# Performance work log

Hardware: AMD Instinct MI355X
Metric: run time of the kernel (lower is better)

## Reference

```python
import jax, jax.numpy as jnp
import numpy as np
from jax import lax

CONF_THRESH = 0.65
NMS_THRESH = 0.55
EPS = 1e-16


def setup_inputs() -> dict:
    key = jax.random.key(0)
    x = jax.random.uniform(key, (8, 4096, 85), dtype=jnp.float32)
    return {"x": x}


def _xywh2xyxy(b):
    # b: [..., 4] center-x, center-y, w, h -> x1, y1, x2, y2
    cx, cy, w, h = b[..., 0], b[..., 1], b[..., 2], b[..., 3]
    return jnp.stack([cx - w / 2, cy - h / 2, cx + w / 2, cy + h / 2], axis=-1)


def _pairwise_iou(boxes):
    # boxes: [bs, N, 4] in xyxy -> iou: [bs, N, N]
    x1, y1, x2, y2 = boxes[..., 0], boxes[..., 1], boxes[..., 2], boxes[..., 3]
    ix1 = jnp.maximum(x1[:, :, None], x1[:, None, :])
    iy1 = jnp.maximum(y1[:, :, None], y1[:, None, :])
    ix2 = jnp.minimum(x2[:, :, None], x2[:, None, :])
    iy2 = jnp.minimum(y2[:, :, None], y2[:, None, :])
    inter = jnp.clip(ix2 - ix1, 0.0) * jnp.clip(iy2 - iy1, 0.0)
    area = (x2 - x1) * (y2 - y1)
    return inter / (area[:, :, None] + area[:, None, :] - inter + EPS)


def reference(x):
    # x: [bs, N, 5 + nC]
    bs, N, _ = x.shape
    obj = x[..., 4]
    valid = obj > CONF_THRESH                      # foreground filter
    boxes = _xywh2xyxy(x[..., :4])
    max_conf = jnp.max(x[..., 5:], axis=-1)        # per-box best class score
    cls_idx = jnp.argmax(x[..., 5:], axis=-1)

    # sort descending by class confidence (invalid boxes pushed to the end)
    sort_key = jnp.where(valid, max_conf, -jnp.inf)
    order = jnp.argsort(-sort_key, axis=1)         # [bs, N]
    boxes_s = jnp.take_along_axis(boxes, order[..., None], axis=1)
    obj_s = jnp.take_along_axis(obj, order, axis=1)
    conf_s = jnp.take_along_axis(max_conf, order, axis=1)
    cls_s = jnp.take_along_axis(cls_idx, order, axis=1)
    valid_s = jnp.take_along_axis(valid, order, axis=1)

    # candidate suppression matrix: same class AND IoU above threshold
    iou = _pairwise_iou(boxes_s)                   # [bs, N, N]
    same_cls = cls_s[:, :, None] == cls_s[:, None, :]
    sup_mat = (iou > NMS_THRESH) & same_cls        # [bs, N, N]

    # greedy sequential NMS over boxes in descending-score order
    def step(suppressed, xs):
        sup_row, vld, i = xs                       # sup_row: [bs, N], vld: [bs]
        keep_i = vld & ~suppressed[:, i]
        suppressed = suppressed | (keep_i[:, None] & sup_row)
        return suppressed, keep_i

    xs = (jnp.swapaxes(sup_mat, 0, 1), valid_s.T, jnp.arange(N))
    _, keeps = lax.scan(step, jnp.zeros((bs, N), dtype=bool), xs)
    keep = keeps.T                                 # [bs, N]

    # [batch_idx, x1, y1, x2, y2, p_obj, max_conf, cls_idx]; non-kept rows zeroed
    batch_idx = jnp.broadcast_to(
        jnp.arange(bs, dtype=x.dtype)[:, None, None], (bs, N, 1))
    preds = jnp.concatenate(
        [batch_idx, boxes_s, obj_s[..., None], conf_s[..., None],
         cls_s[..., None].astype(x.dtype)], axis=-1)  # [bs, N, 8]
    return preds * keep[..., None].astype(x.dtype)
```

## Files before the change

kernel.cpp:

```cpp
#include <hip/hip_runtime.h>

constexpr int BS = 8;
constexpr int N  = 4096;
constexpr int F  = 85;
constexpr int NC = 80;
constexpr float CONF_T = 0.65f;
constexpr float NMS_T  = 0.55f;
constexpr int MC   = 96;
constexpr int SEGS = 32;
constexpr int SEGR = 128;


__global__ __launch_bounds__(256) void prep_kernel(
        const float* __restrict__ x,
        unsigned long long* __restrict__ gkeys,
        float4* __restrict__ vbox,
        float2* __restrict__ vco,
        int* __restrict__ cntblk,
        float4* __restrict__ out) {
    __shared__ __align__(16) float sx[SEGR * F];
    __shared__ float sbest2[SEGR];
    __shared__ int   sbi2[SEGR];
    __shared__ int   wq[4];
    const int tid = threadIdx.x, blk = blockIdx.x;
    const int row0 = blk * SEGR;
    const float4* src = (const float4*)(x + (size_t)row0 * F);
    float4* dst = (float4*)sx;
    constexpr int NV4 = SEGR * F / 4;
    for (int i = tid; i < NV4; i += 256) dst[i] = src[i];
    out[(size_t)row0 * 2 + tid] = make_float4(0.f, 0.f, 0.f, 0.f);
    __syncthreads();

    const int r = tid & 127, h = tid >> 7;
    float mybest; int mybi;
    {
        const float* p = sx + r * F + 5 + h * 40;
        float best = p[0]; int bi = 0;
        #pragma unroll 8
        for (int c = 1; c < 40; ++c) {
            float v = p[c];
            if (v > best) { best = v; bi = c; }
        }
        mybest = best; mybi = bi + h * 40;
        if (h) { sbest2[r] = best; sbi2[r] = mybi; }
    }
    __syncthreads();

    bool valid = false;
    unsigned long long key = 0;
    if (!h) {
        float b1 = sbest2[r];
        if (b1 > mybest) { mybest = b1; mybi = sbi2[r]; }
        const float* p = sx + r * F;
        float obj = p[4];
        valid = obj > CONF_T;
        const int t = row0 + r;
        if (valid) {
            float cx = p[0], cy = p[1], w = p[2], hh = p[3];
            vbox[t] = make_float4(cx - w * 0.5f, cy - hh * 0.5f,
                                  cx + w * 0.5f, cy + hh * 0.5f);
            vco[t]  = make_float2(obj, mybest);
        }
        key = ((unsigned long long)(~__float_as_uint(mybest)) << 19)
            | ((unsigned long long)(unsigned)(t & (N - 1)) << 7)
            | (unsigned)mybi;
    }
    const int lane = tid & 63, w = tid >> 6;
    unsigned long long mask = __ballot(valid);
    if (lane == 0) wq[w] = __popcll(mask);
    __syncthreads();
    int base = 0;
    for (int i = 0; i < w; ++i) base += wq[i];
    if (valid) {
        int slot = base + __popcll(mask & ((1ull << lane) - 1ull));
        gkeys[((size_t)(blk >> 5) << 12) + ((blk & 31) << 7) + slot] = key;
    }
    if (tid == 0) cntblk[blk] = wq[0] + wq[1];
}

__global__ __launch_bounds__(256) void rank_kernel(
        const unsigned long long* __restrict__ gkeys,
        const float4* __restrict__ vbox,
        const float2* __restrict__ vco,
        const int* __restrict__ cntblk,
        float4* __restrict__ rbox,
        float2* __restrict__ rco,
        int* __restrict__ rcls,
        int* __restrict__ cnt) {
    __shared__ __align__(16) unsigned long long sk[N + 2];
    __shared__ int scnt[SEGS];
    __shared__ int soff[SEGS];
    __shared__ int snv;
    __shared__ int part[256];
    const int b = blockIdx.y, tid = threadIdx.x;
    if (tid < SEGS) {
        int v = cntblk[b * SEGS + tid];
        int xx = v;
        #pragma unroll
        for (int d = 1; d < SEGS; d <<= 1) {
            int y = __shfl_up(xx, d);
            if (tid >= d) xx += y;
        }
        scnt[tid] = v;
        soff[tid] = xx - v;
        if (tid == SEGS - 1) snv = xx;
    }
    __syncthreads();
    const int nv = snv;
    if (blockIdx.x == 0 && tid == 0) cnt[b] = nv;
    const int c0 = blockIdx.x * 64;
    if (c0 >= nv) return;

    const unsigned long long* kb = gkeys + ((size_t)b << 12);
    #pragma unroll 4
    for (int g = tid; g < SEGS * SEGR; g += 256) {
        int s = g >> 7, j = g & 127;
        if (j < scnt[s]) sk[soff[s] + j] = kb[g];
    }
    if (tid == 0) { sk[nv] = ~0ull; sk[nv + 1] = ~0ull; }
    __syncthreads();

    const int li = tid & 63, q = tid >> 6;
    const int bi = c0 + li;
    const bool active = bi < nv;
    const unsigned long long myk = active ? sk[bi] : 0;
    const int P = (nv + 1) >> 1;
    const int j0 = (P * q) >> 2, j1 = (P * (q + 1)) >> 2;
    const ulonglong2* skp = (const ulonglong2*)sk;
    int cr = 0;
    for (int j = j0; j < j1; ++j) {
        ulonglong2 kk = skp[j];
        cr += (kk.x < myk) ? 1 : 0;
        cr += (kk.y < myk) ? 1 : 0;
    }
    part[tid] = cr;
    __syncthreads();
    if (q == 0 && active) {
        int rank = part[li] + part[li + 64] + part[li + 128] + part[li + 192];
        int idx = (int)((myk >> 7) & (N - 1));
        int s = (b << 12) + idx;
        int d = (b << 12) + rank;
        rbox[d] = vbox[s];
        rco[d]  = vco[s];
        rcls[d] = (int)(myk & 127u);
    }
}

__global__ __launch_bounds__(64) void nms_kernel(
        const float4* __restrict__ rbox,
        const float2* __restrict__ rco,
        const int* __restrict__ rcls,
        const int* __restrict__ cnt,
        float4* __restrict__ out) {
    __shared__ float4 sbox[MC];
    __shared__ unsigned short srank[MC];
    __shared__ unsigned char srem[MC];
    const int c = blockIdx.x, b = blockIdx.y, lane = threadIdx.x;
    const int bN = b << 12;
    const int nv = cnt[b];
    constexpr int MAXCH = 32;

    int cv[MAXCH];
    #pragma unroll
    for (int ch = 0; ch < MAXCH; ++ch) {
        int rn = ch * 64 + lane;
        cv[ch] = rcls[bN + (rn < nv ? rn : 0)];
    }
    int n = 0;
    #pragma unroll
    for (int ch = 0; ch < MAXCH; ++ch) {
        int rn = ch * 64 + lane;
        bool member = (rn < nv) && (cv[ch] == c);
        unsigned long long mb = __ballot(member);
        if (member) {
            int pos = n + __popcll(mb & ((1ull << lane) - 1ull));
            if (pos < MC) srank[pos] = (unsigned short)rn;
        }
        n += __popcll(mb);
    }
    for (int base = MAXCH * 64; base < nv; base += 64) {
        int rn = base + lane;
        bool member = (rn < nv) && (rcls[bN + (rn < nv ? rn : 0)] == c);
        unsigned long long mb = __ballot(member);
        if (member) {
            int pos = n + __popcll(mb & ((1ull << lane) - 1ull));
            if (pos < MC) srank[pos] = (unsigned short)rn;
        }
        n += __popcll(mb);
    }
    if (n > MC) n = MC;
    const int m = n;

    for (int i = lane; i < m; i += 64) {
        sbox[i] = rbox[bN + srank[i]];
        srem[i] = 0;
    }

    for (int i = 0; i < m; ++i) {
        if (srem[i]) continue;
        float4 bi4 = sbox[i];
        float ai = (bi4.z - bi4.x) * (bi4.w - bi4.y);
        for (int j = i + 1 + lane; j < m; j += 64) {
            if (!srem[j]) {
                float4 bj = sbox[j];
                float ix1 = fmaxf(bi4.x, bj.x);
                float iy1 = fmaxf(bi4.y, bj.y);
                float ix2 = fminf(bi4.z, bj.z);
                float iy2 = fminf(bi4.w, bj.w);
                float inter = fmaxf(ix2 - ix1, 0.0f) * fmaxf(iy2 - iy1, 0.0f);
                float aj = (bj.z - bj.x) * (bj.w - bj.y);
                float iou = inter / (ai + aj - inter + 1e-16f);
                if (iou > NMS_T) srem[j] = 1;
            }
        }
    }
    for (int j = lane; j < m; j += 64) {
        if (!srem[j]) {
            int rr = srank[j];
            float4 bq = sbox[j];
            float2 oc = rco[bN + rr];
            float4* o = out + (size_t)(bN + rr) * 2;
            o[0] = make_float4((float)b, bq.x, bq.y, bq.z);
            o[1] = make_float4(bq.w, oc.x, oc.y, (float)c);
        }
    }
}

extern "C" void kernel_launch(void* const* d_in, const int* in_sizes, int n_in,
                              void* d_out, int out_size, void* d_ws, size_t ws_size,
                              hipStream_t stream) {
    const float* x = (const float*)d_in[0];
    float4* out = (float4*)d_out;

    char* ws = (char*)d_ws;
    size_t off = 0;
    auto alloc = [&](size_t bytes) { char* p = ws + off; off += (bytes + 255) & ~255ull; return p; };
    unsigned long long* gkeys = (unsigned long long*)alloc(BS * N * 8);
    float4* vbox = (float4*)alloc(BS * N * 16);
    float2* vco  = (float2*)alloc(BS * N * 8);
    int*    cntblk = (int*)alloc(BS * SEGS * 4);
    float4* rbox = (float4*)alloc(BS * N * 16);
    float2* rco  = (float2*)alloc(BS * N * 8);
    int*    rcls = (int*)alloc(BS * N * 4);
    int*    cnt  = (int*)alloc(BS * 4);

    prep_kernel<<<BS * N / SEGR, 256, 0, stream>>>(x, gkeys, vbox, vco, cntblk, out);
    rank_kernel<<<dim3(64, BS), 256, 0, stream>>>(gkeys, vbox, vco, cntblk,
                                                  rbox, rco, rcls, cnt);
    nms_kernel<<<dim3(NC, BS), 64, 0, stream>>>(rbox, rco, rcls, cnt, out);
}
```

Baseline: 91.99 us.

## Shrink prep blocks, shuffle-reduce argmax, and compact keys via per-batch atomics

The prep kernel now handles 32 rows per block, with 8 threads per row doing a shuffle-based argmax, which gives 4x more blocks and removes the shared-memory reduction barriers. Per-segment counts and the prefix scan in rank_kernel are replaced by a wavefront-level atomicAdd on a per-batch counter, so rank_kernel loads a dense key array directly. The cost is an extra memset launch and atomic contention. Key order in the array is now nondeterministic, but ranking by full key comparison keeps the output deterministic.

New measurement: 132.4 us. +44.0%, slower.

```diff
diff --git a/kernel.cpp b/kernel.cpp
--- a/kernel.cpp
+++ b/kernel.cpp
@@ -7,8 +7,8 @@
 constexpr float CONF_T = 0.65f;
 constexpr float NMS_T  = 0.55f;
 constexpr int MC   = 96;
-constexpr int SEGS = 32;
-constexpr int SEGR = 128;
+constexpr int SEGR = 32;
+constexpr int BPB  = N / SEGR;
 
 
 __global__ __launch_bounds__(256) void prep_kernel(
@@ -16,41 +16,42 @@
         unsigned long long* __restrict__ gkeys,
         float4* __restrict__ vbox,
         float2* __restrict__ vco,
-        int* __restrict__ cntblk,
+        int* __restrict__ cnt,
         float4* __restrict__ out) {
     __shared__ __align__(16) float sx[SEGR * F];
-    __shared__ float sbest2[SEGR];
-    __shared__ int   sbi2[SEGR];
-    __shared__ int   wq[4];
     const int tid = threadIdx.x, blk = blockIdx.x;
     const int row0 = blk * SEGR;
+    const int b = blk >> 7;
     const float4* src = (const float4*)(x + (size_t)row0 * F);
     float4* dst = (float4*)sx;
     constexpr int NV4 = SEGR * F / 4;
     for (int i = tid; i < NV4; i += 256) dst[i] = src[i];
-    out[(size_t)row0 * 2 + tid] = make_float4(0.f, 0.f, 0.f, 0.f);
+    if (tid < SEGR * 2)
+        out[(size_t)row0 * 2 + tid] = make_float4(0.f, 0.f, 0.f, 0.f);
     __syncthreads();
 
-    const int r = tid & 127, h = tid >> 7;
-    float mybest; int mybi;
+    const int r = tid >> 3, h = tid & 7;
+    float best; int bidx;
     {
-        const float* p = sx + r * F + 5 + h * 40;
-        float best = p[0]; int bi = 0;
-        #pragma unroll 8
-        for (int c = 1; c < 40; ++c) {
+        const float* p = sx + r * F + 5 + h * 10;
+        float bv = p[0]; int bi = 0;
+        #pragma unroll
+        for (int c = 1; c < 10; ++c) {
             float v = p[c];
-            if (v > best) { best = v; bi = c; }
-        }
-        mybest = best; mybi = bi + h * 40;
-        if (h) { sbest2[r] = best; sbi2[r] = mybi; }
-    }
-    __syncthreads();
+            if (v > bv) { bv = v; bi = c; }
+        }
+        best = bv; bidx = bi + h * 10;
+    }
+    #pragma unroll
+    for (int d = 1; d < 8; d <<= 1) {
+        float ov = __shfl_xor(best, d);
+        int   oi = __shfl_xor(bidx, d);
+        if (ov > best || (ov == best && oi < bidx)) { best = ov; bidx = oi; }
+    }
 
     bool valid = false;
     unsigned long long key = 0;
-    if (!h) {
-        float b1 = sbest2[r];
-        if (b1 > mybest) { mybest = b1; mybi = sbi2[r]; }
+    if (h == 0) {
         const float* p = sx + r * F;
         float obj = p[4];
         valid = obj > CONF_T;
@@ -59,64 +60,43 @@
             float cx = p[0], cy = p[1], w = p[2], hh = p[3];
             vbox[t] = make_float4(cx - w * 0.5f, cy - hh * 0.5f,
                                   cx + w * 0.5f, cy + hh * 0.5f);
-            vco[t]  = make_float2(obj, mybest);
-        }
-        key = ((unsigned long long)(~__float_as_uint(mybest)) << 19)
-            | ((unsigned long long)(unsigned)(t & (N - 1)) << 7)
-            | (unsigned)mybi;
-    }
-    const int lane = tid & 63, w = tid >> 6;
+            vco[t]  = make_float2(obj, best);
+            key = ((unsigned long long)(~__float_as_uint(best)) << 19)
+                | ((unsigned long long)(unsigned)(t & (N - 1)) << 7)
+                | (unsigned)bidx;
+        }
+    }
     unsigned long long mask = __ballot(valid);
-    if (lane == 0) wq[w] = __popcll(mask);
-    __syncthreads();
-    int base = 0;
-    for (int i = 0; i < w; ++i) base += wq[i];
-    if (valid) {
-        int slot = base + __popcll(mask & ((1ull << lane) - 1ull));
-        gkeys[((size_t)(blk >> 5) << 12) + ((blk & 31) << 7) + slot] = key;
-    }
-    if (tid == 0) cntblk[blk] = wq[0] + wq[1];
+    int nw = __popcll(mask);
+    if (nw) {
+        const int lane = tid & 63;
+        int base;
+        if (lane == 0) base = atomicAdd(&cnt[b], nw);
+        base = __shfl(base, 0);
+        if (valid) {
+            int slot = base + __popcll(mask & ((1ull << lane) - 1ull));
+            gkeys[((size_t)b << 12) + slot] = key;
+        }
+    }
 }
 
 __global__ __launch_bounds__(256) void rank_kernel(
         const unsigned long long* __restrict__ gkeys,
         const float4* __restrict__ vbox,
         const float2* __restrict__ vco,
-        const int* __restrict__ cntblk,
+        const int* __restrict__ cnt,
         float4* __restrict__ rbox,
         float2* __restrict__ rco,
-        int* __restrict__ rcls,
-        int* __restrict__ cnt) {
+        int* __restrict__ rcls) {
     __shared__ __align__(16) unsigned long long sk[N + 2];
-    __shared__ int scnt[SEGS];
-    __shared__ int soff[SEGS];
-    __shared__ int snv;
     __shared__ int part[256];
     const int b = blockIdx.y, tid = threadIdx.x;
-    if (tid < SEGS) {
-        int v = cntblk[b * SEGS + tid];
-        int xx = v;
-        #pragma unroll
-        for (int d = 1; d < SEGS; d <<= 1) {
-            int y = __shfl_up(xx, d);
-            if (tid >= d) xx += y;
-        }
-        scnt[tid] = v;
-        soff[tid] = xx - v;
-        if (tid == SEGS - 1) snv = xx;
-    }
-    __syncthreads();
-    const int nv = snv;
-    if (blockIdx.x == 0 && tid == 0) cnt[b] = nv;
+    const int nv = cnt[b];
     const int c0 = blockIdx.x * 64;
     if (c0 >= nv) return;
 
     const unsigned long long* kb = gkeys + ((size_t)b << 12);
-    #pragma unroll 4
-    for (int g = tid; g < SEGS * SEGR; g += 256) {
-        int s = g >> 7, j = g & 127;
-        if (j < scnt[s]) sk[soff[s] + j] = kb[g];
-    }
+    for (int i = tid; i < nv; i += 256) sk[i] = kb[i];
     if (tid == 0) { sk[nv] = ~0ull; sk[nv + 1] = ~0ull; }
     __syncthreads();
 
@@ -238,14 +218,14 @@
     unsigned long long* gkeys = (unsigned long long*)alloc(BS * N * 8);
     float4* vbox = (float4*)alloc(BS * N * 16);
     float2* vco  = (float2*)alloc(BS * N * 8);
-    int*    cntblk = (int*)alloc(BS * SEGS * 4);
     float4* rbox = (float4*)alloc(BS * N * 16);
     float2* rco  = (float2*)alloc(BS * N * 8);
     int*    rcls = (int*)alloc(BS * N * 4);
     int*    cnt  = (int*)alloc(BS * 4);
 
-    prep_kernel<<<BS * N / SEGR, 256, 0, stream>>>(x, gkeys, vbox, vco, cntblk, out);
-    rank_kernel<<<dim3(64, BS), 256, 0, stream>>>(gkeys, vbox, vco, cntblk,
-                                                  rbox, rco, rcls, cnt);
+    hipMemsetAsync(cnt, 0, BS * sizeof(int), stream);
+    prep_kernel<<<BS * N / SEGR, 256, 0, stream>>>(x, gkeys, vbox, vco, cnt, out);
+    rank_kernel<<<dim3(64, BS), 256, 0, stream>>>(gkeys, vbox, vco, cnt,
+                                                  rbox, rco, rcls);
     nms_kernel<<<dim3(NC, BS), 64, 0, stream>>>(rbox, rco, rcls, cnt, out);
 }
```
